# Kernel tuning notes

Hardware: AMD Instinct MI355X
Metric: run time of the kernel (lower is better)

## Reference

```python
import jax, jax.numpy as jnp
import numpy as np

N_QUBITS = 16
N_LAYERS = 4
BATCH = 512


def _apply_1q(state, U, q):
    # state: (B,) + (2,)*n complex64; U: (B,2,2) complex64; acts on qubit q
    s = jnp.moveaxis(state, 1 + q, 1)
    s = jnp.einsum('bij,bj...->bi...', U, s)
    return jnp.moveaxis(s, 1, 1 + q)


def _ry(a):
    # batched RY(a): (B,2,2)
    c = jnp.cos(a / 2)
    s = jnp.sin(a / 2)
    U = jnp.stack([jnp.stack([c, -s], -1), jnp.stack([s, c], -1)], -2)
    return U.astype(jnp.complex64)


def _rot(phi, theta, omega):
    # PennyLane Rot(phi,theta,omega) = RZ(omega) @ RY(theta) @ RZ(phi)
    c = jnp.cos(theta / 2)
    s = jnp.sin(theta / 2)
    U = jnp.stack([
        jnp.stack([jnp.exp(-0.5j * (phi + omega)) * c, -jnp.exp(0.5j * (phi - omega)) * s]),
        jnp.stack([jnp.exp(-0.5j * (phi - omega)) * s, jnp.exp(0.5j * (phi + omega)) * c]),
    ])
    return U.astype(jnp.complex64)


def _cnot(state, ctrl, tgt):
    # flip target axis where control == 1
    s = jnp.moveaxis(state, (1 + ctrl, 1 + tgt), (1, 2))
    s = jnp.concatenate([s[:, 0:1], s[:, 1:2, ::-1]], axis=1)
    return jnp.moveaxis(s, (1, 2), (1 + ctrl, 1 + tgt))


def setup_inputs() -> dict:
    key = jax.random.key(0)
    k1, k2 = jax.random.split(key)
    inputs = jax.random.normal(k1, (BATCH, N_QUBITS), dtype=jnp.float32)
    params = jax.random.normal(k2, (N_LAYERS, N_QUBITS, 3), dtype=jnp.float32)
    return {"inputs": inputs, "params": params}


def reference(inputs, params):
    B = inputs.shape[0]
    n = N_QUBITS
    # |0...0> statevector, one per batch element
    state = jnp.zeros((B, 2 ** n), jnp.complex64).at[:, 0].set(1.0)
    state = state.reshape((B,) + (2,) * n)
    # RY feature map (angle differs per batch element)
    for i in range(n):
        state = _apply_1q(state, _ry(inputs[:, i]), i)
    # variational layers: Rot on each wire, then CNOT chain
    for layer in range(N_LAYERS):
        for i in range(n):
            U = _rot(params[layer, i, 0], params[layer, i, 1], params[layer, i, 2])
            state = _apply_1q(state, jnp.broadcast_to(U, (B, 2, 2)), i)
        for i in range(n - 1):
            state = _cnot(state, i, i + 1)
    # <Z> on wire 0
    probs = jnp.abs(state.reshape(B, 2, -1)) ** 2
    return (probs[:, 0].sum(-1) - probs[:, 1].sum(-1)).astype(jnp.float32)
```

## Files before the change

kernel.cpp:

```cpp
#include <hip/hip_runtime.h>


#define NQ 16

__device__ __forceinline__ float2 cmul(float2 a, float2 b){
    return make_float2(a.x*b.x - a.y*b.y, a.x*b.y + a.y*b.x);
}
__device__ __forceinline__ float2 cmulc(float2 a, float2 b){
    return make_float2(a.x*b.x + a.y*b.y, a.x*b.y - a.y*b.x);
}
__device__ __forceinline__ void cfma(float2& acc, float2 a, float2 b){
    acc.x = fmaf(a.x, b.x, fmaf(-a.y, b.y, acc.x));
    acc.y = fmaf(a.x, b.y, fmaf( a.y, b.x, acc.y));
}
__device__ __forceinline__ void cfmac(float2& acc, float2 a, float2 b){
    acc.x = fmaf(a.x, b.x, fmaf( a.y, b.y, acc.x));
    acc.y = fmaf(a.x, b.y, fmaf(-a.y, b.x, acc.y));
}
__device__ __forceinline__ float2 shfl2(float2 v, int bidx){
    int x = __builtin_amdgcn_ds_bpermute(bidx, __float_as_int(v.x));
    int y = __builtin_amdgcn_ds_bpermute(bidx, __float_as_int(v.y));
    return make_float2(__int_as_float(x), __int_as_float(y));
}

__device__ __forceinline__ void make_rot(const float* __restrict__ params, int L, int q, float u[8]){
    const float* pp = params + (L*NQ + q)*3;
    float phi = pp[0], th = pp[1], om = pp[2];
    float s, c;     sincosf(0.5f*th, &s, &c);
    float sap, cap; sincosf(0.5f*(phi+om), &sap, &cap);
    float sam, cam; sincosf(0.5f*(phi-om), &sam, &cam);
    u[0] =  c*cap; u[1] = -c*sap;
    u[2] = -s*cam; u[3] = -s*sam;
    u[4] =  s*cam; u[5] = -s*sam;
    u[6] =  c*cap; u[7] =  c*sap;
}
__device__ __forceinline__ void fuse_ry(float a, float u[8]){
    float sa, ca; sincosf(0.5f*a, &sa, &ca);
    float f0r =  u[0]*ca + u[2]*sa, f0i =  u[1]*ca + u[3]*sa;
    float f1r = -u[0]*sa + u[2]*ca, f1i = -u[1]*sa + u[3]*ca;
    float g0r =  u[4]*ca + u[6]*sa, g0i =  u[5]*ca + u[7]*sa;
    float g1r = -u[4]*sa + u[6]*ca, g1i = -u[5]*sa + u[7]*ca;
    u[0]=f0r; u[1]=f0i; u[2]=f1r; u[3]=f1i; u[4]=g0r; u[5]=g0i; u[6]=g1r; u[7]=g1i;
}

__device__ __forceinline__ void load_col(const float2* __restrict__ p, float2 dst[8]){
    const float4* q = (const float4*)p;
    #pragma unroll
    for (int h = 0; h < 4; ++h) {
        float4 f = q[h];
        dst[2*h]   = make_float2(f.x, f.y);
        dst[2*h+1] = make_float2(f.z, f.w);
    }
}

__launch_bounds__(64)
__global__ void qmps_kernel(const float* __restrict__ inputs,
                            const float* __restrict__ params,
                            float* __restrict__ out)
{
    __shared__ __align__(16) float2 U[3][NQ][2][2];
    __shared__ __align__(16) float2 v[NQ][2];
    __shared__ __align__(16) float2 wc[14][2][8][10];
    __shared__ __align__(16) float2 B0s[2][8];
    __shared__ __align__(16) float2 r15s[8][2];

    const int t = threadIdx.x;
    const int b = blockIdx.x;

    if (t < 48) {
        int l = t >> 4, q = t & 15;
        float u[8]; make_rot(params, l+1, q, u);
        U[l][q][0][0] = make_float2(u[0],u[1]); U[l][q][0][1] = make_float2(u[2],u[3]);
        U[l][q][1][0] = make_float2(u[4],u[5]); U[l][q][1][1] = make_float2(u[6],u[7]);
    } else {
        int q = t - 48;
        float u[8]; make_rot(params, 0, q, u);
        fuse_ry(inputs[b*NQ + q], u);
        v[q][0] = make_float2(u[0],u[1]);
        v[q][1] = make_float2(u[4],u[5]);
    }
    __syncthreads();

    #pragma unroll 4
    for (int kk = 0; kk < 28; ++kk) {
        int e     = t + (kk << 6);
        int ws    = e >> 7;
        int idx   = e & 127;
        int alpha = idx & 7, beta = (idx >> 3) & 7, m = (idx >> 6) & 1;
        int site  = ws + 1;
        int uu = (site <= 7) ? alpha : beta;
        int dd = (site <= 7) ? beta  : alpha;
        int c1 = uu & 1, c2 = (uu >> 1) & 1, c3 = (uu >> 2) & 1;
        int d1 = dd & 1, d2 = (dd >> 1) & 1, d3 = (dd >> 2) & 1;
        float2 val = cmul(U[2][site][m][d3],
                     cmul(U[1][site][d3^c3][d2],
                     cmul(U[0][site][d2^c2][d1], v[site][d1^c1])));
        wc[ws][m][beta][alpha] = val;
    }
    if (t < 16) {
        int jj = t >> 3, ap = t & 7;
        int d1 = ap & 1, d2 = (ap>>1)&1, d3 = (ap>>2)&1;
        B0s[jj][ap] = cmul(U[2][0][jj][d3],
                      cmul(U[1][0][d3][d2],
                      cmul(U[0][0][d2][d1], v[0][d1])));
    } else if (t < 32) {
        int t2 = t - 16;
        int a = t2 >> 1, k = t2 & 1;
        int c1 = a & 1, c2 = (a>>1)&1, c3 = (a>>2)&1;
        float2 in1[2], in2[2];
        #pragma unroll
        for (int s2 = 0; s2 < 2; ++s2) {
            float2 acc = make_float2(0.f, 0.f);
            #pragma unroll
            for (int s1 = 0; s1 < 2; ++s1) cfma(acc, U[0][15][s2^c2][s1], v[15][s1^c1]);
            in1[s2] = acc;
        }
        #pragma unroll
        for (int s3 = 0; s3 < 2; ++s3) {
            float2 acc = make_float2(0.f, 0.f);
            #pragma unroll
            for (int s2 = 0; s2 < 2; ++s2) cfma(acc, U[1][15][s3^c3][s2], in1[s2]);
            in2[s3] = acc;
        }
        float2 acc = make_float2(0.f, 0.f);
        #pragma unroll
        for (int s3 = 0; s3 < 2; ++s3) cfma(acc, U[2][15][k][s3], in2[s3]);
        r15s[a][k] = acc;
    }
    __syncthreads();

    const int i = t >> 3, j = t & 7;
    float2 LamL0, LamL1, LamR0, LamR1;
    {
        LamL0 = cmulc(B0s[0][i], B0s[0][j]);
        float2 l1 = cmulc(B0s[1][i], B0s[1][j]);
        LamL1 = make_float2(-l1.x, -l1.y);
        float2 r = cmulc(r15s[i][0], r15s[j][0]);
        cfmac(r, r15s[i][1], r15s[j][1]);
        LamR0 = r; LamR1 = r;
    }

    const int iA0 = (t << 2) & 0xE0;
    const int jB0 = (t & 7) << 2;

    #pragma unroll 1
    for (int st = 0; st < 7; ++st) {
        const int sL = st, sR = 13 - st;
        float2 W1L[2][8], W2L[2][8], W1R[2][8], W2R[2][8];
        #pragma unroll
        for (int m = 0; m < 2; ++m) {
            load_col(&wc[sL][m][j][0], W1L[m]);
            load_col(&wc[sL][m][i][0], W2L[m]);
            load_col(&wc[sR][m][j][0], W1R[m]);
            load_col(&wc[sR][m][i][0], W2R[m]);
        }
        float2 PL00 = make_float2(0.f,0.f), PL01 = make_float2(0.f,0.f);
        float2 PL10 = make_float2(0.f,0.f), PL11 = make_float2(0.f,0.f);
        float2 PR00 = make_float2(0.f,0.f), PR01 = make_float2(0.f,0.f);
        float2 PR10 = make_float2(0.f,0.f), PR11 = make_float2(0.f,0.f);
        #pragma unroll
        for (int k = 0; k < 8; ++k) {
            const int iA = iA0 | (k << 2);
            float2 a0 = shfl2(LamL0, iA);
            float2 a1 = shfl2(LamL1, iA);
            float2 b0 = shfl2(LamR0, iA);
            float2 b1 = shfl2(LamR1, iA);
            cfma(PL00, a0, W1L[0][k]); cfma(PL01, a0, W1L[1][k]);
            cfma(PL10, a1, W1L[0][k]); cfma(PL11, a1, W1L[1][k]);
            cfma(PR00, b0, W1R[0][k]); cfma(PR01, b0, W1R[1][k]);
            cfma(PR10, b1, W1R[0][k]); cfma(PR11, b1, W1R[1][k]);
        }
        float2 nL0 = make_float2(0.f,0.f), nL1 = make_float2(0.f,0.f);
        float2 nR0 = make_float2(0.f,0.f), nR1 = make_float2(0.f,0.f);
        #pragma unroll
        for (int k = 0; k < 8; ++k) {
            const int iB = jB0 | (k << 5);
            float2 p00 = shfl2(PL00, iB);
            float2 p01 = shfl2(PL01, iB);
            float2 p10 = shfl2(PL10, iB);
            float2 p11 = shfl2(PL11, iB);
            cfmac(nL0, W2L[0][k], p00); cfmac(nL0, W2L[1][k], p11);
            cfmac(nL1, W2L[1][k], p01); cfmac(nL1, W2L[0][k], p10);
            float2 q00 = shfl2(PR00, iB);
            float2 q01 = shfl2(PR01, iB);
            float2 q10 = shfl2(PR10, iB);
            float2 q11 = shfl2(PR11, iB);
            cfmac(nR0, W2R[0][k], q00); cfmac(nR0, W2R[1][k], q11);
            cfmac(nR1, W2R[1][k], q01); cfmac(nR1, W2R[0][k], q10);
        }
        LamL0 = nL0; LamL1 = nL1; LamR0 = nR0; LamR1 = nR1;
    }

    float m = LamL0.x*LamR0.x - LamL0.y*LamR0.y
            + LamL1.x*LamR1.x - LamL1.y*LamR1.y;
    #pragma unroll
    for (int off = 32; off > 0; off >>= 1) m += __shfl_down(m, off, 64);
    if (t == 0) out[b] = m;
}

extern "C" void kernel_launch(void* const* d_in, const int* in_sizes, int n_in,
                              void* d_out, int out_size, void* d_ws, size_t ws_size,
                              hipStream_t stream) {
    (void)n_in; (void)out_size; (void)d_ws; (void)ws_size;
    const float* inputs = (const float*)d_in[0];
    const float* params = (const float*)d_in[1];
    float* out = (float*)d_out;
    const int B = in_sizes[0] / NQ;
    qmps_kernel<<<B, 64, 0, stream>>>(inputs, params, out);
}
```

Measured before the change: 72.35 us.

## Split left and right transfer-matrix sweeps across two wavefronts per block

The block grows from one wavefront to two. Wave 0 runs the left environment contraction and wave 1 runs the right one, replacing the single wave that interleaved both. The final overlap is exchanged through shared memory with one extra barrier, and the per-site tensor build is spread over 128 threads. This halves the serial dependent shuffle and FMA chain per wave and lowers register pressure, at the cost of more threads per block and a sync at the end. The st loop is also now fully unrolled.

```diff
diff --git a/kernel.cpp b/kernel.cpp
--- a/kernel.cpp
+++ b/kernel.cpp
@@ -53,7 +53,7 @@
     }
 }
 
-__launch_bounds__(64)
+__launch_bounds__(128)
 __global__ void qmps_kernel(const float* __restrict__ inputs,
                             const float* __restrict__ params,
                             float* __restrict__ out)
@@ -63,17 +63,20 @@
     __shared__ __align__(16) float2 wc[14][2][8][10];
     __shared__ __align__(16) float2 B0s[2][8];
     __shared__ __align__(16) float2 r15s[8][2];
-
-    const int t = threadIdx.x;
-    const int b = blockIdx.x;
+    __shared__ __align__(16) float2 XL[2][8][10];
+
+    const int t    = threadIdx.x;
+    const int b    = blockIdx.x;
+    const int wv   = t >> 6;
+    const int lane = t & 63;
 
     if (t < 48) {
         int l = t >> 4, q = t & 15;
         float u[8]; make_rot(params, l+1, q, u);
         U[l][q][0][0] = make_float2(u[0],u[1]); U[l][q][0][1] = make_float2(u[2],u[3]);
         U[l][q][1][0] = make_float2(u[4],u[5]); U[l][q][1][1] = make_float2(u[6],u[7]);
-    } else {
-        int q = t - 48;
+    } else if (t >= 64 && t < 80) {
+        int q = t - 64;
         float u[8]; make_rot(params, 0, q, u);
         fuse_ry(inputs[b*NQ + q], u);
         v[q][0] = make_float2(u[0],u[1]);
@@ -81,12 +84,10 @@
     }
     __syncthreads();
 
-    #pragma unroll 4
-    for (int kk = 0; kk < 28; ++kk) {
-        int e     = t + (kk << 6);
-        int ws    = e >> 7;
-        int idx   = e & 127;
-        int alpha = idx & 7, beta = (idx >> 3) & 7, m = (idx >> 6) & 1;
+    #pragma unroll 2
+    for (int kk = 0; kk < 14; ++kk) {
+        int ws    = kk;
+        int alpha = t & 7, beta = (t >> 3) & 7, m = (t >> 6) & 1;
         int site  = ws + 1;
         int uu = (site <= 7) ? alpha : beta;
         int dd = (site <= 7) ? beta  : alpha;
@@ -97,14 +98,15 @@
                      cmul(U[0][site][d2^c2][d1], v[site][d1^c1])));
         wc[ws][m][beta][alpha] = val;
     }
-    if (t < 16) {
-        int jj = t >> 3, ap = t & 7;
+    if (t >= 64 && t < 80) {
+        int t2 = t - 64;
+        int jj = t2 >> 3, ap = t2 & 7;
         int d1 = ap & 1, d2 = (ap>>1)&1, d3 = (ap>>2)&1;
         B0s[jj][ap] = cmul(U[2][0][jj][d3],
                       cmul(U[1][0][d3][d2],
                       cmul(U[0][0][d2][d1], v[0][d1])));
-    } else if (t < 32) {
-        int t2 = t - 16;
+    } else if (t >= 80 && t < 96) {
+        int t2 = t - 80;
         int a = t2 >> 1, k = t2 & 1;
         int c1 = a & 1, c2 = (a>>1)&1, c3 = (a>>2)&1;
         float2 in1[2], in2[2];
@@ -129,73 +131,69 @@
     }
     __syncthreads();
 
-    const int i = t >> 3, j = t & 7;
-    float2 LamL0, LamL1, LamR0, LamR1;
-    {
-        LamL0 = cmulc(B0s[0][i], B0s[0][j]);
+    const int i = lane >> 3, j = lane & 7;
+
+    float2 L0, L1;
+    if (wv == 0) {
+        L0 = cmulc(B0s[0][i], B0s[0][j]);
         float2 l1 = cmulc(B0s[1][i], B0s[1][j]);
-        LamL1 = make_float2(-l1.x, -l1.y);
+        L1 = make_float2(-l1.x, -l1.y);
+    } else {
         float2 r = cmulc(r15s[i][0], r15s[j][0]);
         cfmac(r, r15s[i][1], r15s[j][1]);
-        LamR0 = r; LamR1 = r;
-    }
-
-    const int iA0 = (t << 2) & 0xE0;
-    const int jB0 = (t & 7) << 2;
-
-    #pragma unroll 1
+        L0 = r; L1 = r;
+    }
+
+    const int iA0 = (lane & 0x38) << 2;
+    const int jB0 = (lane & 7) << 2;
+
+    #pragma unroll
     for (int st = 0; st < 7; ++st) {
-        const int sL = st, sR = 13 - st;
-        float2 W1L[2][8], W2L[2][8], W1R[2][8], W2R[2][8];
+        const int slot = wv ? (13 - st) : st;
+        float2 W1[2][8], W2[2][8];
         #pragma unroll
         for (int m = 0; m < 2; ++m) {
-            load_col(&wc[sL][m][j][0], W1L[m]);
-            load_col(&wc[sL][m][i][0], W2L[m]);
-            load_col(&wc[sR][m][j][0], W1R[m]);
-            load_col(&wc[sR][m][i][0], W2R[m]);
-        }
-        float2 PL00 = make_float2(0.f,0.f), PL01 = make_float2(0.f,0.f);
-        float2 PL10 = make_float2(0.f,0.f), PL11 = make_float2(0.f,0.f);
-        float2 PR00 = make_float2(0.f,0.f), PR01 = make_float2(0.f,0.f);
-        float2 PR10 = make_float2(0.f,0.f), PR11 = make_float2(0.f,0.f);
+            load_col(&wc[slot][m][j][0], W1[m]);
+            load_col(&wc[slot][m][i][0], W2[m]);
+        }
+        float2 P00 = make_float2(0.f,0.f), P01 = make_float2(0.f,0.f);
+        float2 P10 = make_float2(0.f,0.f), P11 = make_float2(0.f,0.f);
         #pragma unroll
         for (int k = 0; k < 8; ++k) {
             const int iA = iA0 | (k << 2);
-            float2 a0 = shfl2(LamL0, iA);
-            float2 a1 = shfl2(LamL1, iA);
-            float2 b0 = shfl2(LamR0, iA);
-            float2 b1 = shfl2(LamR1, iA);
-            cfma(PL00, a0, W1L[0][k]); cfma(PL01, a0, W1L[1][k]);
-            cfma(PL10, a1, W1L[0][k]); cfma(PL11, a1, W1L[1][k]);
-            cfma(PR00, b0, W1R[0][k]); cfma(PR01, b0, W1R[1][k]);
-            cfma(PR10, b1, W1R[0][k]); cfma(PR11, b1, W1R[1][k]);
-        }
-        float2 nL0 = make_float2(0.f,0.f), nL1 = make_float2(0.f,0.f);
-        float2 nR0 = make_float2(0.f,0.f), nR1 = make_float2(0.f,0.f);
+            float2 a0 = shfl2(L0, iA);
+            float2 a1 = shfl2(L1, iA);
+            cfma(P00, a0, W1[0][k]); cfma(P01, a0, W1[1][k]);
+            cfma(P10, a1, W1[0][k]); cfma(P11, a1, W1[1][k]);
+        }
+        float2 n0 = make_float2(0.f,0.f), n1 = make_float2(0.f,0.f);
         #pragma unroll
         for (int k = 0; k < 8; ++k) {
             const int iB = jB0 | (k << 5);
-            float2 p00 = shfl2(PL00, iB);
-            float2 p01 = shfl2(PL01, iB);
-            float2 p10 = shfl2(PL10, iB);
-            float2 p11 = shfl2(PL11, iB);
-            cfmac(nL0, W2L[0][k], p00); cfmac(nL0, W2L[1][k], p11);
-            cfmac(nL1, W2L[1][k], p01); cfmac(nL1, W2L[0][k], p10);
-            float2 q00 = shfl2(PR00, iB);
-            float2 q01 = shfl2(PR01, iB);
-            float2 q10 = shfl2(PR10, iB);
-            float2 q11 = shfl2(PR11, iB);
-            cfmac(nR0, W2R[0][k], q00); cfmac(nR0, W2R[1][k], q11);
-            cfmac(nR1, W2R[1][k], q01); cfmac(nR1, W2R[0][k], q10);
-        }
-        LamL0 = nL0; LamL1 = nL1; LamR0 = nR0; LamR1 = nR1;
-    }
-
-    float m = LamL0.x*LamR0.x - LamL0.y*LamR0.y
-            + LamL1.x*LamR1.x - LamL1.y*LamR1.y;
-    #pragma unroll
-    for (int off = 32; off > 0; off >>= 1) m += __shfl_down(m, off, 64);
-    if (t == 0) out[b] = m;
+            float2 p00 = shfl2(P00, iB);
+            float2 p01 = shfl2(P01, iB);
+            float2 p10 = shfl2(P10, iB);
+            float2 p11 = shfl2(P11, iB);
+            cfmac(n0, W2[0][k], p00); cfmac(n0, W2[1][k], p11);
+            cfmac(n1, W2[1][k], p01); cfmac(n1, W2[0][k], p10);
+        }
+        L0 = n0; L1 = n1;
+    }
+
+    if (wv == 0) {
+        XL[0][i][j] = L0;
+        XL[1][i][j] = L1;
+    }
+    __syncthreads();
+    if (wv == 1) {
+        float2 A0 = XL[0][i][j];
+        float2 A1 = XL[1][i][j];
+        float m = A0.x*L0.x - A0.y*L0.y
+                + A1.x*L1.x - A1.y*L1.y;
+        #pragma unroll
+        for (int off = 32; off > 0; off >>= 1) m += __shfl_down(m, off, 64);
+        if (lane == 0) out[b] = m;
+    }
 }
 
 extern "C" void kernel_launch(void* const* d_in, const int* in_sizes, int n_in,
@@ -206,5 +204,5 @@
     const float* params = (const float*)d_in[1];
     float* out = (float*)d_out;
     const int B = in_sizes[0] / NQ;
-    qmps_kernel<<<B, 64, 0, stream>>>(inputs, params, out);
-}
+    qmps_kernel<<<B, 128, 0, stream>>>(inputs, params, out);
+}
```

Result: faster. 68.26 us (-5.6%).
